# Kernel tuning notes

Hardware: AMD Instinct MI355X
Metric: run time of the kernel (lower is better)

Reference implementation:

```python
import jax, jax.numpy as jnp
import numpy as np

N_NODES = 100000
D_FEAT = 128            # per-embedding width; concat of 4 -> 512
INPUT_DIM = 4 * D_FEAT
HIDDEN_DIM = 64
N_SAMPLES = 250000


def _glorot(key, fan_in, fan_out):
    r = np.sqrt(6.0 / fan_in).astype(np.float32)
    return jax.random.uniform(key, (fan_in, fan_out), minval=-r, maxval=r, dtype=jnp.float32)


def setup_inputs() -> dict:
    key = jax.random.key(0)
    k1, k2, k3, k4, k5 = jax.random.split(key, 5)
    input1 = jax.random.normal(k1, (N_NODES, D_FEAT), dtype=jnp.float32)
    input2 = jax.random.normal(k2, (N_NODES, D_FEAT), dtype=jnp.float32)
    train_sample = jax.random.randint(k3, (N_SAMPLES, 2), 0, N_NODES, dtype=jnp.int64)
    w1 = _glorot(k4, INPUT_DIM, HIDDEN_DIM)
    b1 = jnp.zeros((HIDDEN_DIM,), dtype=jnp.float32)
    w2 = _glorot(k5, HIDDEN_DIM, 1)
    return {"input1": input1, "input2": input2, "train_sample": train_sample,
            "w1": w1, "b1": b1, "w2": w2}


def reference(input1, input2, train_sample, w1, b1, w2):
    src = train_sample[:, 0]
    dst = train_sample[:, 1]
    # four gathers + concat -> [E, 4*D_FEAT]
    h = jnp.concatenate([input1[src], input1[dst], input2[src], input2[dst]], axis=1)
    x = jax.nn.relu(h @ w1 + b1)          # [E, HIDDEN_DIM]
    return x @ w2                          # [E, 1]
```

## Files before the change

### kernel.cpp

```cpp
#include <hip/hip_runtime.h>
#include <hip/hip_bf16.h>

#define NN  100000
#define DF  128
#define HD  64
#define NS  250000


typedef __attribute__((ext_vector_type(8))) short bfrag;
typedef __attribute__((ext_vector_type(4))) float ffrag;

__device__ __forceinline__ unsigned short bf16bits(float f) {
    __hip_bfloat16 b = __float2bfloat16(f);
    return *(unsigned short*)&b;
}
__device__ __forceinline__ unsigned pack2(float a, float b) {
    return (unsigned)bf16bits(a) | ((unsigned)bf16bits(b) << 16);
}
__device__ __forceinline__ float bflo(unsigned u) {
    union { unsigned i; float f; } c; c.i = u << 16; return c.f;
}
__device__ __forceinline__ float bfhi(unsigned u) {
    union { unsigned i; float f; } c; c.i = u & 0xffff0000u; return c.f;
}
__device__ __forceinline__ void barrier_lgkm_only() {
    __builtin_amdgcn_s_waitcnt(0xC07F);
    __builtin_amdgcn_s_barrier();
}

__global__ __launch_bounds__(256) void prep_w1_kernel(
    const float* __restrict__ w1, const float* __restrict__ w2,
    unsigned short* __restrict__ Bf, unsigned short* __restrict__ w2bf)
{
    const int gid = blockIdx.x * 256 + threadIdx.x;
    if (gid >= 4096) {
        const int j = gid - 4096;
        if (j < HD) w2bf[j] = bf16bits(w2[j]);
        return;
    }
    const int lane = gid & 63;
    const int ks   = (gid >> 6) & 7;
    const int tn   = gid >> 9;

    const int n     = tn * 16 + (lane & 15);
    const int kbase = ks * 32 + (lane >> 4) * 8;
    const int col   = n & 63;

    uint4 u;
    unsigned p[4];
    #pragma unroll
    for (int jp = 0; jp < 4; ++jp) {
        float v[2];
        #pragma unroll
        for (int h = 0; h < 2; ++h) {
            const int k = kbase + jp * 2 + h;
            const int row = ((k >= 128) ? 256 : 0) + ((n >= 64) ? 128 : 0) + (k & 127);
            v[h] = w1[(size_t)row * HD + col];
        }
        p[jp] = pack2(v[0], v[1]);
    }
    u.x = p[0]; u.y = p[1]; u.z = p[2]; u.w = p[3];
    *(uint4*)(Bf + (size_t)gid * 8) = u;
}

#define NTILE 2
#define NBLK  (NN / (16 * NTILE))

__global__ __launch_bounds__(256) void node_gemm_mfma(
    const float* __restrict__ in1,
    const float* __restrict__ in2,
    const unsigned short* __restrict__ Bf,
    const float* __restrict__ b1,
    unsigned short* __restrict__ Pn)
{
    __shared__ unsigned short smem[8192 + 4 * 576];

    const int t    = threadIdx.x;
    const int lane = t & 63;
    const int w    = t >> 6;

    bfrag bfr[2][8];
    #pragma unroll
    for (int ti = 0; ti < 2; ++ti) {
        const int tn = w * 2 + ti;
        #pragma unroll
        for (int ks = 0; ks < 8; ++ks)
            bfr[ti][ks] = *(const bfrag*)(Bf + ((size_t)(tn * 8 + ks) * 64 + lane) * 8);
    }
    float badd[2];
    #pragma unroll
    for (int ti = 0; ti < 2; ++ti) {
        const int nc = w * 32 + ti * 16 + (lane & 15);
        badd[ti] = (w < 2) ? b1[nc] : 0.f;
    }

    int ldsoff[4];
    #pragma unroll
    for (int i = 0; i < 4; ++i) {
        const int p  = (i & 1) * 256 + t;
        const int m  = p >> 5;
        const int c  = p & 31;
        const int k  = ((i >> 1) ? 128 : 0) + c * 4;
        const int ks = k >> 5;
        const int g  = (k >> 3) & 3;
        const int l  = m + 16 * g;
        ldsoff[i] = ks * 512 + ((l * 8) ^ (g << 3)) + (k & 7);
    }
    const int lane_off = (lane * 8) ^ ((lane >> 4) << 3);

    const int tile0 = blockIdx.x * NTILE;

    float4 cur[4], nxt[4];
    {
        const float* a1 = in1 + (size_t)tile0 * 16 * DF;
        const float* a2 = in2 + (size_t)tile0 * 16 * DF;
        cur[0] = *(const float4*)(a1 + t * 4);
        cur[1] = *(const float4*)(a1 + 1024 + t * 4);
        cur[2] = *(const float4*)(a2 + t * 4);
        cur[3] = *(const float4*)(a2 + 1024 + t * 4);
    }

    #pragma unroll
    for (int it = 0; it < NTILE; ++it) {
        const int m0 = (tile0 + it) * 16;

        if (it + 1 < NTILE) {
            const float* a1 = in1 + (size_t)(m0 + 16) * DF;
            const float* a2 = in2 + (size_t)(m0 + 16) * DF;
            nxt[0] = *(const float4*)(a1 + t * 4);
            nxt[1] = *(const float4*)(a1 + 1024 + t * 4);
            nxt[2] = *(const float4*)(a2 + t * 4);
            nxt[3] = *(const float4*)(a2 + 1024 + t * 4);
        }

        unsigned short* abuf = &smem[(it & 1) * 4096];
        #pragma unroll
        for (int i = 0; i < 4; ++i) {
            uint2 u;
            u.x = pack2(cur[i].x, cur[i].y);
            u.y = pack2(cur[i].z, cur[i].w);
            *(uint2*)(&abuf[ldsoff[i]]) = u;
        }

        barrier_lgkm_only();

        ffrag acc[2] = {{0.f, 0.f, 0.f, 0.f}, {0.f, 0.f, 0.f, 0.f}};
        #pragma unroll
        for (int ks = 0; ks < 8; ++ks) {
            const bfrag af = *(const bfrag*)(&abuf[ks * 512 + lane_off]);
            acc[0] = __builtin_amdgcn_mfma_f32_16x16x32_bf16(af, bfr[0][ks], acc[0], 0, 0, 0);
            acc[1] = __builtin_amdgcn_mfma_f32_16x16x32_bf16(af, bfr[1][ks], acc[1], 0, 0, 0);
        }

        {
            unsigned short* ep = &smem[8192 + w * 576];
            const int col = lane & 15;
            const int rq  = lane >> 4;
            #pragma unroll
            for (int ti = 0; ti < 2; ++ti) {
                #pragma unroll
                for (int reg = 0; reg < 4; ++reg)
                    ep[(rq * 4 + reg) * 36 + ti * 16 + col] =
                        bf16bits(acc[ti][reg] + badd[ti]);
            }
            const int rowm = lane >> 2;
            const int seg  = lane & 3;
            const uint4 u = *(const uint4*)(&ep[rowm * 36 + seg * 8]);
            *(uint4*)(Pn + (size_t)(m0 + rowm) * 128 + w * 32 + seg * 8) = u;
        }

        #pragma unroll
        for (int i = 0; i < 4; ++i) cur[i] = nxt[i];
    }
}

#define EBLK   1024
#define EPASS  4
__global__ __launch_bounds__(256) void edge_mlp_kernel(
    const unsigned short* __restrict__ Pn,
    const int*   __restrict__ ts,
    const unsigned short* __restrict__ w2bf,
    float* __restrict__ out)
{
    const int t = threadIdx.x;
    const int q = t & 3;
    const int g = t >> 2;

    const uint4 w0 = *(const uint4*)(w2bf + q * 16);
    const uint4 w1v = *(const uint4*)(w2bf + q * 16 + 8);

    const int2* ts2 = (const int2*)ts;

    int sr = blockIdx.x * 64 + g;
    int2 e = ts2[min(sr, NS - 1)];

    #pragma unroll
    for (int p = 0; p < EPASS; ++p) {
        const unsigned short* up = Pn + (size_t)e.x * 128 + q * 16;
        const unsigned short* vp = Pn + (size_t)e.y * 128 + 64 + q * 16;
        const uint4 u0 = *(const uint4*)(up);
        const uint4 u1 = *(const uint4*)(up + 8);
        const uint4 v0 = *(const uint4*)(vp);
        const uint4 v1 = *(const uint4*)(vp + 8);

        const int sr_n = sr + EBLK * 64;
        int2 e_n;
        if (p + 1 < EPASS) e_n = ts2[min(sr_n, NS - 1)];

        float acc = 0.f, x;
        x = bflo(u0.x) + bflo(v0.x); x = x > 0.f ? x : 0.f; acc += x * bflo(w0.x);
        x = bfhi(u0.x) + bfhi(v0.x); x = x > 0.f ? x : 0.f; acc += x * bfhi(w0.x);
        x = bflo(u0.y) + bflo(v0.y); x = x > 0.f ? x : 0.f; acc += x * bflo(w0.y);
        x = bfhi(u0.y) + bfhi(v0.y); x = x > 0.f ? x : 0.f; acc += x * bfhi(w0.y);
        x = bflo(u0.z) + bflo(v0.z); x = x > 0.f ? x : 0.f; acc += x * bflo(w0.z);
        x = bfhi(u0.z) + bfhi(v0.z); x = x > 0.f ? x : 0.f; acc += x * bfhi(w0.z);
        x = bflo(u0.w) + bflo(v0.w); x = x > 0.f ? x : 0.f; acc += x * bflo(w0.w);
        x = bfhi(u0.w) + bfhi(v0.w); x = x > 0.f ? x : 0.f; acc += x * bfhi(w0.w);
        x = bflo(u1.x) + bflo(v1.x); x = x > 0.f ? x : 0.f; acc += x * bflo(w1v.x);
        x = bfhi(u1.x) + bfhi(v1.x); x = x > 0.f ? x : 0.f; acc += x * bfhi(w1v.x);
        x = bflo(u1.y) + bflo(v1.y); x = x > 0.f ? x : 0.f; acc += x * bflo(w1v.y);
        x = bfhi(u1.y) + bfhi(v1.y); x = x > 0.f ? x : 0.f; acc += x * bfhi(w1v.y);
        x = bflo(u1.z) + bflo(v1.z); x = x > 0.f ? x : 0.f; acc += x * bflo(w1v.z);
        x = bfhi(u1.z) + bfhi(v1.z); x = x > 0.f ? x : 0.f; acc += x * bfhi(w1v.z);
        x = bflo(u1.w) + bflo(v1.w); x = x > 0.f ? x : 0.f; acc += x * bflo(w1v.w);
        x = bfhi(u1.w) + bfhi(v1.w); x = x > 0.f ? x : 0.f; acc += x * bfhi(w1v.w);

        acc += __shfl_xor(acc, 1);
        acc += __shfl_xor(acc, 2);
        if (q == 0 && sr < NS) out[sr] = acc;

        sr = sr_n;
        e  = e_n;
    }
}

extern "C" void kernel_launch(void* const* d_in, const int* in_sizes, int n_in,
                              void* d_out, int out_size, void* d_ws, size_t ws_size,
                              hipStream_t stream) {
    const float* in1 = (const float*)d_in[0];
    const float* in2 = (const float*)d_in[1];
    const int*   ts  = (const int*)  d_in[2];
    const float* w1  = (const float*)d_in[3];
    const float* b1  = (const float*)d_in[4];
    const float* w2  = (const float*)d_in[5];
    float* out = (float*)d_out;

    unsigned short* Pn = (unsigned short*)d_ws;
    const size_t Pbytes = (size_t)NN * 128 * sizeof(unsigned short);
    unsigned short* Bf;
    unsigned short* w2bf;
    if (ws_size >= Pbytes + 65536 + 128) {
        Bf   = (unsigned short*)((char*)d_ws + Pbytes);
        w2bf = (unsigned short*)((char*)d_ws + Pbytes + 65536);
    } else {
        Bf   = (unsigned short*)d_out;
        w2bf = (unsigned short*)((char*)d_out + 65536);
    }

    prep_w1_kernel<<<17, 256, 0, stream>>>(w1, w2, Bf, w2bf);
    node_gemm_mfma<<<NBLK, 256, 0, stream>>>(in1, in2, Bf, b1, Pn);
    edge_mlp_kernel<<<EBLK, 256, 0, stream>>>(Pn, ts, w2bf, out);
}
```

Baseline: 146.3 us.

## Make node GEMM persistent with per-wave tiles and W1 staged in LDS

The node-projection GEMM now runs as a persistent grid of 512 blocks. Each wave owns a 16-row tile and computes all 128 output columns, reading the W1 fragments from LDS, which every block stages once at start. A-fragments are built directly from registers loaded from global memory, removing the LDS round-trip for A and the per-tile barrier. The next tile is prefetched into registers during the MFMAs. In exchange it uses more registers (16 float4 plus 8 accumulators) and a 64KB LDS footprint, which can lower occupancy, and each lane's global loads are less coalesced.

Result: no change. 146.9 us (+0.4%).

```diff
diff --git a/kernel.cpp b/kernel.cpp
--- a/kernel.cpp
+++ b/kernel.cpp
@@ -26,6 +26,14 @@
 __device__ __forceinline__ void barrier_lgkm_only() {
     __builtin_amdgcn_s_waitcnt(0xC07F);
     __builtin_amdgcn_s_barrier();
+}
+__device__ __forceinline__ bfrag make_frag(const float4& a, const float4& b) {
+    union { bfrag f; unsigned u[4]; } c;
+    c.u[0] = pack2(a.x, a.y);
+    c.u[1] = pack2(a.z, a.w);
+    c.u[2] = pack2(b.x, b.y);
+    c.u[3] = pack2(b.z, b.w);
+    return c.f;
 }
 
 __global__ __launch_bounds__(256) void prep_w1_kernel(
@@ -63,8 +71,9 @@
     *(uint4*)(Bf + (size_t)gid * 8) = u;
 }
 
-#define NTILE 2
-#define NBLK  (NN / (16 * NTILE))
+#define GBLK   512
+#define NWAVE  (GBLK * 4)
+#define NTILES (NN / 16)
 
 __global__ __launch_bounds__(256) void node_gemm_mfma(
     const float* __restrict__ in1,
@@ -73,104 +82,99 @@
     const float* __restrict__ b1,
     unsigned short* __restrict__ Pn)
 {
-    __shared__ unsigned short smem[8192 + 4 * 576];
+    __shared__ unsigned short smem[32768 + 4 * 576];
 
     const int t    = threadIdx.x;
     const int lane = t & 63;
     const int w    = t >> 6;
 
-    bfrag bfr[2][8];
+    const int m    = lane & 15;
+    const int koff = (lane >> 4) * 8;
+
+    int mt = blockIdx.x * 4 + w;
+
+    float4 cur[16];
+    if (mt < NTILES) {
+        const float* r1 = in1 + (size_t)(mt * 16 + m) * DF + koff;
+        const float* r2 = in2 + (size_t)(mt * 16 + m) * DF + koff;
+        #pragma unroll
+        for (int s = 0; s < 4; ++s) {
+            cur[s * 2]     = *(const float4*)(r1 + s * 32);
+            cur[s * 2 + 1] = *(const float4*)(r1 + s * 32 + 4);
+            cur[8 + s * 2] = *(const float4*)(r2 + s * 32);
+            cur[9 + s * 2] = *(const float4*)(r2 + s * 32 + 4);
+        }
+    }
+
+    {
+        const uint4* src = (const uint4*)Bf;
+        uint4* dst = (uint4*)smem;
+        #pragma unroll
+        for (int i = 0; i < 16; ++i)
+            dst[t + i * 256] = src[t + i * 256];
+    }
+
+    float badd[4];
     #pragma unroll
-    for (int ti = 0; ti < 2; ++ti) {
-        const int tn = w * 2 + ti;
-        #pragma unroll
-        for (int ks = 0; ks < 8; ++ks)
-            bfr[ti][ks] = *(const bfrag*)(Bf + ((size_t)(tn * 8 + ks) * 64 + lane) * 8);
-    }
-    float badd[2];
-    #pragma unroll
-    for (int ti = 0; ti < 2; ++ti) {
-        const int nc = w * 32 + ti * 16 + (lane & 15);
-        badd[ti] = (w < 2) ? b1[nc] : 0.f;
-    }
-
-    int ldsoff[4];
-    #pragma unroll
-    for (int i = 0; i < 4; ++i) {
-        const int p  = (i & 1) * 256 + t;
-        const int m  = p >> 5;
-        const int c  = p & 31;
-        const int k  = ((i >> 1) ? 128 : 0) + c * 4;
-        const int ks = k >> 5;
-        const int g  = (k >> 3) & 3;
-        const int l  = m + 16 * g;
-        ldsoff[i] = ks * 512 + ((l * 8) ^ (g << 3)) + (k & 7);
-    }
-    const int lane_off = (lane * 8) ^ ((lane >> 4) << 3);
-
-    const int tile0 = blockIdx.x * NTILE;
-
-    float4 cur[4], nxt[4];
-    {
-        const float* a1 = in1 + (size_t)tile0 * 16 * DF;
-        const float* a2 = in2 + (size_t)tile0 * 16 * DF;
-        cur[0] = *(const float4*)(a1 + t * 4);
-        cur[1] = *(const float4*)(a1 + 1024 + t * 4);
-        cur[2] = *(const float4*)(a2 + t * 4);
-        cur[3] = *(const float4*)(a2 + 1024 + t * 4);
-    }
-
-    #pragma unroll
-    for (int it = 0; it < NTILE; ++it) {
-        const int m0 = (tile0 + it) * 16;
-
-        if (it + 1 < NTILE) {
-            const float* a1 = in1 + (size_t)(m0 + 16) * DF;
-            const float* a2 = in2 + (size_t)(m0 + 16) * DF;
-            nxt[0] = *(const float4*)(a1 + t * 4);
-            nxt[1] = *(const float4*)(a1 + 1024 + t * 4);
-            nxt[2] = *(const float4*)(a2 + t * 4);
-            nxt[3] = *(const float4*)(a2 + 1024 + t * 4);
-        }
-
-        unsigned short* abuf = &smem[(it & 1) * 4096];
-        #pragma unroll
-        for (int i = 0; i < 4; ++i) {
-            uint2 u;
-            u.x = pack2(cur[i].x, cur[i].y);
-            u.y = pack2(cur[i].z, cur[i].w);
-            *(uint2*)(&abuf[ldsoff[i]]) = u;
-        }
-
-        barrier_lgkm_only();
-
-        ffrag acc[2] = {{0.f, 0.f, 0.f, 0.f}, {0.f, 0.f, 0.f, 0.f}};
+    for (int nt = 0; nt < 4; ++nt) badd[nt] = b1[nt * 16 + m];
+
+    barrier_lgkm_only();
+
+    unsigned short* ep = &smem[32768 + w * 576];
+
+    for (; mt < NTILES; mt += NWAVE) {
+        bfrag af[8];
+        #pragma unroll
+        for (int s = 0; s < 4; ++s) {
+            af[s]     = make_frag(cur[s * 2],     cur[s * 2 + 1]);
+            af[4 + s] = make_frag(cur[8 + s * 2], cur[9 + s * 2]);
+        }
+
+        const int mtn = mt + NWAVE;
+        if (mtn < NTILES) {
+            const float* r1 = in1 + (size_t)(mtn * 16 + m) * DF + koff;
+            const float* r2 = in2 + (size_t)(mtn * 16 + m) * DF + koff;
+            #pragma unroll
+            for (int s = 0; s < 4; ++s) {
+                cur[s * 2]     = *(const float4*)(r1 + s * 32);
+                cur[s * 2 + 1] = *(const float4*)(r1 + s * 32 + 4);
+                cur[8 + s * 2] = *(const float4*)(r2 + s * 32);
+                cur[9 + s * 2] = *(const float4*)(r2 + s * 32 + 4);
+            }
+        }
+
+        ffrag acc[8];
+        #pragma unroll
+        for (int nt = 0; nt < 8; ++nt) acc[nt] = ffrag{0.f, 0.f, 0.f, 0.f};
+
         #pragma unroll
         for (int ks = 0; ks < 8; ++ks) {
-            const bfrag af = *(const bfrag*)(&abuf[ks * 512 + lane_off]);
-            acc[0] = __builtin_amdgcn_mfma_f32_16x16x32_bf16(af, bfr[0][ks], acc[0], 0, 0, 0);
-            acc[1] = __builtin_amdgcn_mfma_f32_16x16x32_bf16(af, bfr[1][ks], acc[1], 0, 0, 0);
-        }
-
-        {
-            unsigned short* ep = &smem[8192 + w * 576];
-            const int col = lane & 15;
-            const int rq  = lane >> 4;
             #pragma unroll
-            for (int ti = 0; ti < 2; ++ti) {
+            for (int nt = 0; nt < 8; ++nt) {
+                const bfrag bf = *(const bfrag*)(&smem[((nt * 8 + ks) * 64 + lane) * 8]);
+                acc[nt] = __builtin_amdgcn_mfma_f32_16x16x32_bf16(af[ks], bf, acc[nt], 0, 0, 0);
+            }
+        }
+
+        const int m0   = mt * 16;
+        const int col  = lane & 15;
+        const int rq   = lane >> 4;
+        const int rowm = lane >> 2;
+        const int seg  = lane & 3;
+        #pragma unroll
+        for (int p = 0; p < 4; ++p) {
+            #pragma unroll
+            for (int h = 0; h < 2; ++h) {
+                const int nt = p * 2 + h;
                 #pragma unroll
-                for (int reg = 0; reg < 4; ++reg)
-                    ep[(rq * 4 + reg) * 36 + ti * 16 + col] =
-                        bf16bits(acc[ti][reg] + badd[ti]);
+                for (int reg = 0; reg < 4; ++reg) {
+                    const float v = acc[nt][reg] + ((nt < 4) ? badd[nt] : 0.f);
+                    ep[(rq * 4 + reg) * 36 + h * 16 + col] = bf16bits(v);
+                }
             }
-            const int rowm = lane >> 2;
-            const int seg  = lane & 3;
             const uint4 u = *(const uint4*)(&ep[rowm * 36 + seg * 8]);
-            *(uint4*)(Pn + (size_t)(m0 + rowm) * 128 + w * 32 + seg * 8) = u;
-        }
-
-        #pragma unroll
-        for (int i = 0; i < 4; ++i) cur[i] = nxt[i];
+            *(uint4*)(Pn + (size_t)(m0 + rowm) * 128 + p * 32 + seg * 8) = u;
+        }
     }
 }
 
@@ -258,6 +262,6 @@
     }
 
     prep_w1_kernel<<<17, 256, 0, stream>>>(w1, w2, Bf, w2bf);
-    node_gemm_mfma<<<NBLK, 256, 0, stream>>>(in1, in2, Bf, b1, Pn);
+    node_gemm_mfma<<<GBLK, 256, 0, stream>>>(in1, in2, Bf, b1, Pn);
     edge_mlp_kernel<<<EBLK, 256, 0, stream>>>(Pn, ts, w2bf, out);
 }
```
